# Optimization experiments

Measured on AMD Instinct MI355X. Metric: run time of the kernel, lower is better.

Reference implementation:

```python
import jax, jax.numpy as jnp
import numpy as np

NUM_HEADS = 12


def get_rel_pos(q_size, k_size, rel_pos):
    # rel_pos: (2*max(q,k)-1, C). Here q_size==k_size so no interpolation needed.
    q_coords = jnp.arange(q_size)[:, None] * max(k_size / q_size, 1.0)
    k_coords = jnp.arange(k_size)[None, :] * max(q_size / k_size, 1.0)
    rel = (q_coords - k_coords) + (k_size - 1) * max(q_size / k_size, 1.0)
    return rel_pos[rel.astype(jnp.int32)]  # (q_size, k_size, C)


def add_decomposed_rel_pos(attn, q, rel_pos_h, rel_pos_w, q_size, k_size):
    q_h, q_w = q_size
    k_h, k_w = k_size
    Rh = get_rel_pos(q_h, k_h, rel_pos_h)  # (q_h,k_h,C)
    Rw = get_rel_pos(q_w, k_w, rel_pos_w)  # (q_w,k_w,C)
    B, _, C = q.shape  # B = num_heads * batch
    r_q = q.reshape(B, q_h, q_w, C)
    rel_h = jnp.einsum('bhwc,hkc->bhwk', r_q, Rh)  # (B,q_h,q_w,k_h)
    rel_w = jnp.einsum('bhwc,wkc->bhwk', r_q, Rw)  # (B,q_h,q_w,k_w)
    attn = attn.reshape(B, q_h, q_w, k_h, k_w)
    attn = attn + rel_h[:, :, :, :, None] + rel_w[:, :, :, None, :]
    return attn.reshape(B, q_h * q_w, k_h * k_w)


def setup_inputs() -> dict:
    key = jax.random.key(0)
    ks = jax.random.split(key, 7)
    B, H, W, dim = 128, 14, 14, 768
    head_dim = dim // NUM_HEADS
    return {
        'x': jax.random.normal(ks[0], (B, H, W, dim), dtype=jnp.float32),
        'qkv_w': jax.random.normal(ks[1], (dim, 3 * dim), dtype=jnp.float32) * 0.02,
        'qkv_b': jax.random.normal(ks[2], (3 * dim,), dtype=jnp.float32) * 0.02,
        'proj_w': jax.random.normal(ks[3], (dim, dim), dtype=jnp.float32) * 0.02,
        'proj_b': jax.random.normal(ks[4], (dim,), dtype=jnp.float32) * 0.02,
        'rel_pos_h': jax.random.normal(ks[5], (2 * H - 1, head_dim), dtype=jnp.float32) * 0.02,
        'rel_pos_w': jax.random.normal(ks[6], (2 * W - 1, head_dim), dtype=jnp.float32) * 0.02,
    }


def reference(x, qkv_w, qkv_b, proj_w, proj_b, rel_pos_h, rel_pos_w):
    B, H, W, dim = x.shape
    nh = NUM_HEADS
    hd = dim // nh
    scale = hd ** -0.5
    L = H * W
    # qkv projection: (B,H,W,3*dim) -> (3, nh*B, L, hd)
    qkv = x.reshape(B, L, dim) @ qkv_w + qkv_b
    qkv = qkv.reshape(B, L, 3, nh, hd)
    qkv = jnp.transpose(qkv, (2, 3, 0, 1, 4)).reshape(3, nh * B, L, hd)
    q, k, v = qkv[0], qkv[1], qkv[2]
    attn = jnp.einsum('bqc,bkc->bqk', q * scale, k)  # (nh*B, L, L)
    attn = add_decomposed_rel_pos(attn, q, rel_pos_h, rel_pos_w, (H, W), (H, W))
    attn = jax.nn.softmax(attn, axis=-1)
    out = jnp.einsum('bqk,bkc->bqc', attn, v)  # (nh*B, L, hd)
    out = out.reshape(nh, B, H, W, hd)
    out = jnp.transpose(out, (1, 2, 3, 0, 4)).reshape(B, H, W, dim)
    return out @ proj_w + proj_b
```

## Files before the change

kernel.cpp:

```cpp
#include <hip/hip_runtime.h>
#include <stdint.h>

typedef unsigned short u16;
typedef __bf16 bf16x8 __attribute__((ext_vector_type(8)));
typedef u16 u16x8 __attribute__((ext_vector_type(8)));
typedef float f32x4 __attribute__((ext_vector_type(4)));

#define MFMA16(a,b,c) __builtin_amdgcn_mfma_f32_16x16x32_bf16((a),(b),(c),0,0,0)
#define GLOAD16(gp, lp) __builtin_amdgcn_global_load_lds( \
    (const __attribute__((address_space(1))) void*)(gp), \
    (__attribute__((address_space(3))) void*)(lp), 16, 0, 0)

__device__ __forceinline__ u16 f2bf(float f) {
  union { float f; uint32_t u; } v; v.f = f;
  return (u16)((v.u + 0x7FFFu + ((v.u >> 16) & 1u)) >> 16);
}
__device__ __forceinline__ float bits2f(uint32_t u) {
  union { uint32_t u; float f; } v; v.u = u; return v.f;
}

__global__ void k_cvt(const float* __restrict__ in, u16* __restrict__ out, int n4) {
  int i = blockIdx.x * 256 + threadIdx.x;
  int stride = gridDim.x * 256;
  for (; i < n4; i += stride) {
    float4 v = reinterpret_cast<const float4*>(in)[i];
    ushort4 o;
    o.x = f2bf(v.x); o.y = f2bf(v.y); o.z = f2bf(v.z); o.w = f2bf(v.w);
    reinterpret_cast<ushort4*>(out)[i] = o;
  }
}

__global__ void k_transpose(const float* __restrict__ in, u16* __restrict__ out, int R, int C) {
  __shared__ float t[32][33];
  int tx = threadIdx.x & 31, ty = threadIdx.x >> 5;
  int c0 = blockIdx.x * 32, r0 = blockIdx.y * 32;
  #pragma unroll
  for (int i = 0; i < 4; i++)
    t[ty + i*8][tx] = in[(size_t)(r0 + ty + i*8) * C + (c0 + tx)];
  __syncthreads();
  #pragma unroll
  for (int i = 0; i < 4; i++)
    out[(size_t)(c0 + ty + i*8) * R + (r0 + tx)] = f2bf(t[tx][ty + i*8]);
}

template<int KDIM>
__device__ __forceinline__ void gemm_core(
    const u16* __restrict__ A, const u16* __restrict__ BT,
    int mt, int nt, f32x4 acc[4][4], u16* As, u16* Bs)
{
  int tid = threadIdx.x, lane = tid & 63, w = tid >> 6;
  int g = lane >> 4, c4 = lane & 15;
  int wr = w >> 1, wc = w & 1;
  int srow = lane >> 2;
  int pslot = (lane & 3) ^ ((lane >> 3) & 3);
  int rsel = g ^ ((c4 >> 1) & 3);
  const size_t abase = (size_t)(mt * 128) * KDIM;
  const size_t bbase = (size_t)(nt * 128) * KDIM;
  for (int kt = 0; kt < KDIM / 32; kt++) {
    __syncthreads();
    #pragma unroll
    for (int cc = 0; cc < 2; cc++) {
      int cid = w * 2 + cc;
      int row = cid * 16 + srow;
      GLOAD16(A + abase + (size_t)row * KDIM + kt * 32 + pslot * 8, As + cid * 512);
      GLOAD16(BT + bbase + (size_t)row * KDIM + kt * 32 + pslot * 8, Bs + cid * 512);
    }
    __syncthreads();
    bf16x8 af[4], bfv[4];
    #pragma unroll
    for (int f = 0; f < 4; f++) {
      af[f]  = *(const bf16x8*)(As + (wr * 64 + f * 16 + c4) * 32 + rsel * 8);
      bfv[f] = *(const bf16x8*)(Bs + (wc * 64 + f * 16 + c4) * 32 + rsel * 8);
    }
    #pragma unroll
    for (int fr = 0; fr < 4; fr++)
      #pragma unroll
      for (int fc = 0; fc < 4; fc++)
        acc[fr][fc] = MFMA16(af[fr], bfv[fc], acc[fr][fc]);
  }
}

__global__ __launch_bounds__(256, 3) void k_qkv_gemm(
    const u16* __restrict__ A, const u16* __restrict__ BT, const float* __restrict__ bias,
    u16* __restrict__ qo, u16* __restrict__ ko, u16* __restrict__ vo)
{
  __shared__ u16 As[128 * 32], Bs[128 * 32];
  int bid = blockIdx.x;
  int nt = bid % 18, mt = bid / 18;
  f32x4 z = {0.f, 0.f, 0.f, 0.f};
  f32x4 acc[4][4];
  #pragma unroll
  for (int i = 0; i < 4; i++)
    #pragma unroll
    for (int j = 0; j < 4; j++) acc[i][j] = z;
  gemm_core<768>(A, BT, mt, nt, acc, As, Bs);

  int tid = threadIdx.x, lane = tid & 63, w = tid >> 6;
  int g = lane >> 4, c4 = lane & 15;
  int wr = w >> 1, wc = w & 1;

  u16* dstA[4]; int ccA[4]; float bsA[4]; int hbA[4];
  #pragma unroll
  for (int fc = 0; fc < 4; fc++) {
    int n0 = nt * 128 + wc * 64 + fc * 16;
    int i3 = n0 / 768;
    int r = n0 - i3 * 768;
    dstA[fc] = (i3 == 0) ? qo : (i3 == 1) ? ko : vo;
    hbA[fc] = (r >> 6) * 128;
    ccA[fc] = (r & 63) + c4;
    bsA[fc] = bias[n0 + c4];
  }
  #pragma unroll
  for (int fr = 0; fr < 4; fr++) {
    #pragma unroll
    for (int j = 0; j < 4; j++) {
      int m = mt * 128 + wr * 64 + fr * 16 + g * 4 + j;
      int bb = m / 196;
      int ll = m - bb * 196;
      #pragma unroll
      for (int fc = 0; fc < 4; fc++) {
        dstA[fc][(size_t)((hbA[fc] + bb) * 196 + ll) * 64 + ccA[fc]] =
            f2bf(acc[fr][fc][j] + bsA[fc]);
      }
    }
  }
}

__global__ __launch_bounds__(256, 3) void k_proj_gemm(
    const u16* __restrict__ A, const u16* __restrict__ BT, const float* __restrict__ bias,
    float* __restrict__ out)
{
  __shared__ u16 As[128 * 32], Bs[128 * 32];
  int bid = blockIdx.x;
  int nt = bid % 6, mt = bid / 6;
  f32x4 z = {0.f, 0.f, 0.f, 0.f};
  f32x4 acc[4][4];
  #pragma unroll
  for (int i = 0; i < 4; i++)
    #pragma unroll
    for (int j = 0; j < 4; j++) acc[i][j] = z;
  gemm_core<768>(A, BT, mt, nt, acc, As, Bs);

  int tid = threadIdx.x, lane = tid & 63, w = tid >> 6;
  int g = lane >> 4, c4 = lane & 15;
  int wr = w >> 1, wc = w & 1;
  #pragma unroll
  for (int fc = 0; fc < 4; fc++) {
    int n0 = nt * 128 + wc * 64 + fc * 16 + c4;
    float bs = bias[n0];
    #pragma unroll
    for (int fr = 0; fr < 4; fr++)
      #pragma unroll
      for (int j = 0; j < 4; j++) {
        int m = mt * 128 + wr * 64 + fr * 16 + g * 4 + j;
        out[(size_t)m * 768 + n0] = acc[fr][fc][j] + bs;
      }
  }
}

#define KP 72
#define VP 216
#define PP 136

template<int NT, int KT0, int NMF, int KOFS>
__device__ __forceinline__ void attn_chunk(
    const u16* Kl, const u16* VT, u16* Pw,
    bf16x8 qa0, bf16x8 qa1,
    const uint32_t* ph, const uint32_t* pw,
    const int* qh, const int* qw,
    float* m_run, float* l_run, f32x4* O,
    int g, int c4, int lane)
{
  f32x4 z = {0.f, 0.f, 0.f, 0.f};
  f32x4 S[NT];
  #pragma unroll
  for (int i = 0; i < NT; i++) {
    int key = (KT0 + i) * 16 + c4;
    bf16x8 kb0 = *(const bf16x8*)(Kl + key * KP + g * 8);
    bf16x8 kb1 = *(const bf16x8*)(Kl + key * KP + 32 + g * 8);
    S[i] = MFMA16(qa1, kb1, MFMA16(qa0, kb0, z));
  }
  #pragma unroll
  for (int i = 0; i < NT; i++) {
    int kglob = (KT0 + i) * 16 + c4;
    int kh = kglob / 14;
    int kw = kglob - kh * 14;
    bool valid = (kglob < 196);
    #pragma unroll
    for (int j = 0; j < 4; j++) {
      int ih = qh[j] - kh + 13;
      int iw = qw[j] - kw + 13;
      uint32_t vh = (uint32_t)__builtin_amdgcn_ds_bpermute(((lane & 48) | (ih & 15)) << 2, (int)ph[j]);
      uint32_t vw = (uint32_t)__builtin_amdgcn_ds_bpermute(((lane & 48) | (iw & 15)) << 2, (int)pw[j]);
      float eh = bits2f((ih >= 16) ? (vh & 0xFFFF0000u) : (vh << 16));
      float ew = bits2f((iw >= 16) ? (vw & 0xFFFF0000u) : (vw << 16));
      float s = S[i][j] * 0.125f + eh + ew;
      S[i][j] = valid ? s : -1e30f;
    }
  }
  #pragma unroll
  for (int j = 0; j < 4; j++) {
    float t = S[0][j];
    #pragma unroll
    for (int i = 1; i < NT; i++) t = fmaxf(t, S[i][j]);
    t = fmaxf(t, __shfl_xor(t, 1));
    t = fmaxf(t, __shfl_xor(t, 2));
    t = fmaxf(t, __shfl_xor(t, 4));
    t = fmaxf(t, __shfl_xor(t, 8));
    float mn = fmaxf(m_run[j], t);
    float corr = __expf(m_run[j] - mn);
    m_run[j] = mn;
    l_run[j] *= corr;
    #pragma unroll
    for (int ct = 0; ct < 4; ct++) O[ct][j] *= corr;
  }
  #pragma unroll
  for (int j = 0; j < 4; j++) {
    int prow = (g * 4 + j) * PP;
    float rs = 0.f;
    #pragma unroll
    for (int i = 0; i < NT; i++) {
      float p = __expf(S[i][j] - m_run[j]);
      rs += p;
      Pw[prow + i * 16 + c4] = f2bf(p);
    }
    if (NT == 7) Pw[prow + 112 + c4] = 0;
    rs += __shfl_xor(rs, 1);
    rs += __shfl_xor(rs, 2);
    rs += __shfl_xor(rs, 4);
    rs += __shfl_xor(rs, 8);
    l_run[j] += rs;
  }
  #pragma unroll
  for (int km = 0; km < NMF; km++) {
    bf16x8 pa = *(const bf16x8*)(Pw + c4 * PP + km * 32 + g * 8);
    #pragma unroll
    for (int ct = 0; ct < 4; ct++) {
      bf16x8 vb = *(const bf16x8*)(VT + (ct * 16 + c4) * VP + KOFS + km * 32 + g * 8);
      O[ct] = MFMA16(pa, vb, O[ct]);
    }
  }
}

__global__ __launch_bounds__(256, 2) void k_attn(
    const u16* __restrict__ Q, const u16* __restrict__ Kg, const u16* __restrict__ Vg,
    const u16* __restrict__ RPH, const u16* __restrict__ RPW, u16* __restrict__ Ows)
{
  __shared__ u16 sm[14976 + 13824 + 8704];
  u16* Kl = sm;
  u16* VT = sm + 14976;
  u16* Pl = sm + 14976 + 13824;

  int bh = blockIdx.x;
  int hh = bh >> 7, bb = bh & 127;
  int tid = threadIdx.x, lane = tid & 63, w = tid >> 6;
  int g = lane >> 4, c4 = lane & 15;

  const u16* kbase = Kg + (size_t)bh * (196 * 64);
  const u16* vbase = Vg + (size_t)bh * (196 * 64);
  const u16* qbase = Q + (size_t)bh * (196 * 64);

  for (int ch = tid; ch < 1568; ch += 256) {
    int row = ch >> 3, slot = ch & 7;
    int4 val = *reinterpret_cast<const int4*>(kbase + row * 64 + slot * 8);
    *reinterpret_cast<int4*>(Kl + row * KP + slot * 8) = val;
  }
  for (int i2 = tid; i2 < 12 * KP; i2 += 256) Kl[196 * KP + i2] = 0;
  for (int ch = tid; ch < 784; ch += 256) {
    int kp = ch >> 3, cb = ch & 7;
    int key = kp * 2, cz = cb * 8;
    u16x8 a = *(const u16x8*)(vbase + key * 64 + cz);
    u16x8 b2 = *(const u16x8*)(vbase + (key + 1) * 64 + cz);
    #pragma unroll
    for (int j = 0; j < 8; j++) {
      uint32_t pk = (uint32_t)a[j] | ((uint32_t)b2[j] << 16);
      *reinterpret_cast<uint32_t*>(VT + (cz + j) * VP + key) = pk;
    }
  }
  for (int i2 = tid; i2 < 64 * 20; i2 += 256) {
    int chn = i2 / 20, col = 196 + (i2 - chn * 20);
    VT[chn * VP + col] = 0;
  }
  __syncthreads();

  u16* Pw = Pl + w * (16 * PP);

  for (int qt = w; qt < 13; qt += 4) {
    int qrow = qt * 16 + c4; if (qrow > 195) qrow = 195;
    const u16* qp = qbase + qrow * 64 + g * 8;
    bf16x8 qa0 = *(const bf16x8*)(qp);
    bf16x8 qa1 = *(const bf16x8*)(qp + 32);

    int t1 = 16 + c4; if (t1 > 26) t1 = 26;
    f32x4 z = {0.f, 0.f, 0.f, 0.f};
    f32x4 Eh0 = MFMA16(qa0, *(const bf16x8*)(RPH + c4 * 64 + g * 8), z);
    Eh0 = MFMA16(qa1, *(const bf16x8*)(RPH + c4 * 64 + 32 + g * 8), Eh0);
    f32x4 Eh1 = MFMA16(qa0, *(const bf16x8*)(RPH + t1 * 64 + g * 8), z);
    Eh1 = MFMA16(qa1, *(const bf16x8*)(RPH + t1 * 64 + 32 + g * 8), Eh1);
    f32x4 Ew0 = MFMA16(qa0, *(const bf16x8*)(RPW + c4 * 64 + g * 8), z);
    Ew0 = MFMA16(qa1, *(const bf16x8*)(RPW + c4 * 64 + 32 + g * 8), Ew0);
    f32x4 Ew1 = MFMA16(qa0, *(const bf16x8*)(RPW + t1 * 64 + g * 8), z);
    Ew1 = MFMA16(qa1, *(const bf16x8*)(RPW + t1 * 64 + 32 + g * 8), Ew1);

    uint32_t ph[4], pw[4];
    int qh[4], qw[4];
    #pragma unroll
    for (int j = 0; j < 4; j++) {
      ph[j] = (uint32_t)f2bf(Eh0[j]) | ((uint32_t)f2bf(Eh1[j]) << 16);
      pw[j] = (uint32_t)f2bf(Ew0[j]) | ((uint32_t)f2bf(Ew1[j]) << 16);
      int qi = qt * 16 + g * 4 + j;
      qh[j] = qi / 14;
      qw[j] = qi - qh[j] * 14;
    }

    float m_run[4] = {-3e38f, -3e38f, -3e38f, -3e38f};
    float l_run[4] = {0.f, 0.f, 0.f, 0.f};
    f32x4 O[4] = {z, z, z, z};

    attn_chunk<7, 0, 4, 0>(Kl, VT, Pw, qa0, qa1, ph, pw, qh, qw, m_run, l_run, O, g, c4, lane);
    attn_chunk<6, 7, 3, 112>(Kl, VT, Pw, qa0, qa1, ph, pw, qh, qw, m_run, l_run, O, g, c4, lane);

    #pragma unroll
    for (int j = 0; j < 4; j++) {
      int qi = qt * 16 + g * 4 + j;
      if (qi < 196) {
        float inv = 1.f / l_run[j];
        size_t base = (size_t)(bb * 196 + qi) * 768 + hh * 64;
        #pragma unroll
        for (int ct = 0; ct < 4; ct++)
          Ows[base + ct * 16 + c4] = f2bf(O[ct][j] * inv);
      }
    }
  }
}

extern "C" void kernel_launch(void* const* d_in, const int* in_sizes, int n_in,
                              void* d_out, int out_size, void* d_ws, size_t ws_size,
                              hipStream_t stream) {
  (void)in_sizes; (void)n_in; (void)out_size; (void)ws_size;
  const float* x      = (const float*)d_in[0];
  const float* qkv_w  = (const float*)d_in[1];
  const float* qkv_b  = (const float*)d_in[2];
  const float* proj_w = (const float*)d_in[3];
  const float* proj_b = (const float*)d_in[4];
  const float* rph    = (const float*)d_in[5];
  const float* rpw    = (const float*)d_in[6];
  float* out = (float*)d_out;
  char* ws = (char*)d_ws;

  u16* xb   = (u16*)(ws);
  u16* wT   = (u16*)(ws + 38535168);
  u16* pT   = (u16*)(ws + 42074112);
  u16* rphb = (u16*)(ws + 43253760);
  u16* rpwb = (u16*)(ws + 43257856);
  u16* qws  = (u16*)(ws + 43261952);
  u16* kws  = (u16*)(ws + 81797120);
  u16* vws  = (u16*)(ws + 120332288);
  u16* Ows  = xb;

  k_cvt<<<2048, 256, 0, stream>>>(x, xb, 4816896);
  k_cvt<<<2, 256, 0, stream>>>(rph, rphb, 432);
  k_cvt<<<2, 256, 0, stream>>>(rpw, rpwb, 432);
  k_transpose<<<dim3(72, 24), 256, 0, stream>>>(qkv_w, wT, 768, 2304);
  k_transpose<<<dim3(24, 24), 256, 0, stream>>>(proj_w, pT, 768, 768);
  k_qkv_gemm<<<196 * 18, 256, 0, stream>>>(xb, wT, qkv_b, qws, kws, vws);
  k_attn<<<1536, 256, 0, stream>>>(qws, kws, vws, rphb, rpwb, Ows);
  k_proj_gemm<<<196 * 6, 256, 0, stream>>>(Ows, pT, proj_b, out);
}
```

Before: 313.8 us.

## Restructure attention: fold rel-pos bias into MFMA, transposed S, register P

Rewrites the attention kernel to compute S transposed (keys as rows), folding the decomposed relative-position bias into an extra MFMA using a one-hot key matrix and a per-query rel-pos row in LDS, with the scale pre-applied to K. It drops the online two-chunk softmax for a single-pass max over all 13 key tiles and feeds P straight from registers into the PV MFMA via a permuted V^T layout, removing the LDS P round-trip and the bpermute gathers. K in LDS gets an XOR swizzle, and packed bf16 conversion and vector stores are used for outputs. The QKV and projection GEMMs also remap block indices to change tile scheduling order. In exchange it raises register pressure (13 live S tiles) and rounds the scaled K and the bias to bf16 before use.

```diff
diff --git a/kernel.cpp b/kernel.cpp
--- a/kernel.cpp
+++ b/kernel.cpp
@@ -17,6 +17,19 @@
 }
 __device__ __forceinline__ float bits2f(uint32_t u) {
   union { uint32_t u; float f; } v; v.u = u; return v.f;
+}
+__device__ __forceinline__ uint32_t cvtpk(float lo, float hi) {
+  uint32_t r;
+  asm("v_cvt_pk_bf16_f32 %0, %1, %2" : "=v"(r) : "v"(lo), "v"(hi));
+  return r;
+}
+__device__ __forceinline__ int4 pack8(const u16* v) {
+  int4 r;
+  r.x = (int)((uint32_t)v[0] | ((uint32_t)v[1] << 16));
+  r.y = (int)((uint32_t)v[2] | ((uint32_t)v[3] << 16));
+  r.z = (int)((uint32_t)v[4] | ((uint32_t)v[5] << 16));
+  r.w = (int)((uint32_t)v[6] | ((uint32_t)v[7] << 16));
+  return r;
 }
 
 __global__ void k_cvt(const float* __restrict__ in, u16* __restrict__ out, int n4) {
@@ -85,7 +98,8 @@
     u16* __restrict__ qo, u16* __restrict__ ko, u16* __restrict__ vo)
 {
   __shared__ u16 As[128 * 32], Bs[128 * 32];
-  int bid = blockIdx.x;
+  int bid0 = blockIdx.x;
+  int bid = (bid0 & 7) * 441 + (bid0 >> 3);
   int nt = bid % 18, mt = bid / 18;
   f32x4 z = {0.f, 0.f, 0.f, 0.f};
   f32x4 acc[4][4];
@@ -131,7 +145,8 @@
     float* __restrict__ out)
 {
   __shared__ u16 As[128 * 32], Bs[128 * 32];
-  int bid = blockIdx.x;
+  int bid0 = blockIdx.x;
+  int bid = (bid0 & 7) * 147 + (bid0 >> 3);
   int nt = bid % 6, mt = bid / 6;
   f32x4 z = {0.f, 0.f, 0.f, 0.f};
   f32x4 acc[4][4];
@@ -155,90 +170,6 @@
         int m = mt * 128 + wr * 64 + fr * 16 + g * 4 + j;
         out[(size_t)m * 768 + n0] = acc[fr][fc][j] + bs;
       }
-  }
-}
-
-#define KP 72
-#define VP 216
-#define PP 136
-
-template<int NT, int KT0, int NMF, int KOFS>
-__device__ __forceinline__ void attn_chunk(
-    const u16* Kl, const u16* VT, u16* Pw,
-    bf16x8 qa0, bf16x8 qa1,
-    const uint32_t* ph, const uint32_t* pw,
-    const int* qh, const int* qw,
-    float* m_run, float* l_run, f32x4* O,
-    int g, int c4, int lane)
-{
-  f32x4 z = {0.f, 0.f, 0.f, 0.f};
-  f32x4 S[NT];
-  #pragma unroll
-  for (int i = 0; i < NT; i++) {
-    int key = (KT0 + i) * 16 + c4;
-    bf16x8 kb0 = *(const bf16x8*)(Kl + key * KP + g * 8);
-    bf16x8 kb1 = *(const bf16x8*)(Kl + key * KP + 32 + g * 8);
-    S[i] = MFMA16(qa1, kb1, MFMA16(qa0, kb0, z));
-  }
-  #pragma unroll
-  for (int i = 0; i < NT; i++) {
-    int kglob = (KT0 + i) * 16 + c4;
-    int kh = kglob / 14;
-    int kw = kglob - kh * 14;
-    bool valid = (kglob < 196);
-    #pragma unroll
-    for (int j = 0; j < 4; j++) {
-      int ih = qh[j] - kh + 13;
-      int iw = qw[j] - kw + 13;
-      uint32_t vh = (uint32_t)__builtin_amdgcn_ds_bpermute(((lane & 48) | (ih & 15)) << 2, (int)ph[j]);
-      uint32_t vw = (uint32_t)__builtin_amdgcn_ds_bpermute(((lane & 48) | (iw & 15)) << 2, (int)pw[j]);
-      float eh = bits2f((ih >= 16) ? (vh & 0xFFFF0000u) : (vh << 16));
-      float ew = bits2f((iw >= 16) ? (vw & 0xFFFF0000u) : (vw << 16));
-      float s = S[i][j] * 0.125f + eh + ew;
-      S[i][j] = valid ? s : -1e30f;
-    }
-  }
-  #pragma unroll
-  for (int j = 0; j < 4; j++) {
-    float t = S[0][j];
-    #pragma unroll
-    for (int i = 1; i < NT; i++) t = fmaxf(t, S[i][j]);
-    t = fmaxf(t, __shfl_xor(t, 1));
-    t = fmaxf(t, __shfl_xor(t, 2));
-    t = fmaxf(t, __shfl_xor(t, 4));
-    t = fmaxf(t, __shfl_xor(t, 8));
-    float mn = fmaxf(m_run[j], t);
-    float corr = __expf(m_run[j] - mn);
-    m_run[j] = mn;
-    l_run[j] *= corr;
-    #pragma unroll
-    for (int ct = 0; ct < 4; ct++) O[ct][j] *= corr;
-  }
-  #pragma unroll
-  for (int j = 0; j < 4; j++) {
-    int prow = (g * 4 + j) * PP;
-    float rs = 0.f;
-    #pragma unroll
-    for (int i = 0; i < NT; i++) {
-      float p = __expf(S[i][j] - m_run[j]);
-      rs += p;
-      Pw[prow + i * 16 + c4] = f2bf(p);
-    }
-    if (NT == 7) Pw[prow + 112 + c4] = 0;
-    rs += __shfl_xor(rs, 1);
-    rs += __shfl_xor(rs, 2);
-    rs += __shfl_xor(rs, 4);
-    rs += __shfl_xor(rs, 8);
-    l_run[j] += rs;
-  }
-  #pragma unroll
-  for (int km = 0; km < NMF; km++) {
-    bf16x8 pa = *(const bf16x8*)(Pw + c4 * PP + km * 32 + g * 8);
-    #pragma unroll
-    for (int ct = 0; ct < 4; ct++) {
-      bf16x8 vb = *(const bf16x8*)(VT + (ct * 16 + c4) * VP + KOFS + km * 32 + g * 8);
-      O[ct] = MFMA16(pa, vb, O[ct]);
-    }
   }
 }
 
@@ -246,89 +177,191 @@
     const u16* __restrict__ Q, const u16* __restrict__ Kg, const u16* __restrict__ Vg,
     const u16* __restrict__ RPH, const u16* __restrict__ RPW, u16* __restrict__ Ows)
 {
-  __shared__ u16 sm[14976 + 13824 + 8704];
-  u16* Kl = sm;
-  u16* VT = sm + 14976;
-  u16* Pl = sm + 14976 + 13824;
+  __shared__ u16 K64[208 * 64];
+  __shared__ u16 Krel[208 * 40];
+  __shared__ u16 VT[64 * 232];
+  __shared__ u16 Qrel[4][16 * 40];
 
   int bh = blockIdx.x;
   int hh = bh >> 7, bb = bh & 127;
   int tid = threadIdx.x, lane = tid & 63, w = tid >> 6;
   int g = lane >> 4, c4 = lane & 15;
 
-  const u16* kbase = Kg + (size_t)bh * (196 * 64);
-  const u16* vbase = Vg + (size_t)bh * (196 * 64);
-  const u16* qbase = Q + (size_t)bh * (196 * 64);
-
-  for (int ch = tid; ch < 1568; ch += 256) {
-    int row = ch >> 3, slot = ch & 7;
-    int4 val = *reinterpret_cast<const int4*>(kbase + row * 64 + slot * 8);
-    *reinterpret_cast<int4*>(Kl + row * KP + slot * 8) = val;
-  }
-  for (int i2 = tid; i2 < 12 * KP; i2 += 256) Kl[196 * KP + i2] = 0;
-  for (int ch = tid; ch < 784; ch += 256) {
-    int kp = ch >> 3, cb = ch & 7;
+  const u16* kbase = Kg + (size_t)bh * 12544;
+  const u16* vbase = Vg + (size_t)bh * 12544;
+  const u16* qbase = Q + (size_t)bh * 12544;
+
+  for (int ch = tid; ch < 1664; ch += 256) {
+    int row = ch >> 3, s = ch & 7;
+    u16 outv[8];
+    if (row < 196) {
+      u16x8 v = *(const u16x8*)(kbase + row * 64 + s * 8);
+      #pragma unroll
+      for (int e = 0; e < 8; e++)
+        outv[e] = f2bf(bits2f((uint32_t)v[e] << 16) * 0.125f);
+    } else {
+      #pragma unroll
+      for (int e = 0; e < 8; e++) outv[e] = 0;
+    }
+    *(int4*)(K64 + row * 64 + ((s ^ (row & 7)) * 8)) = pack8(outv);
+  }
+
+  if (tid < 208) {
+    int k = tid;
+    int kh = k / 14, kw2 = k - kh * 14;
+    #pragma unroll
+    for (int s = 0; s < 5; s++) {
+      u16 vals[8];
+      #pragma unroll
+      for (int e = 0; e < 8; e++) {
+        int c = s * 8 + e;
+        u16 x = 0;
+        if (k < 196) {
+          if (c == kh) x = 0x3F80;
+          else if (c == 14 + kw2) x = 0x3F80;
+        } else {
+          if (c == 28) x = 0x3F80;
+        }
+        vals[e] = x;
+      }
+      *(int4*)(Krel + k * 40 + s * 8) = pack8(vals);
+    }
+  }
+
+  for (int i = tid; i < 2048; i += 256) {
+    int chn = i >> 5, c = 192 + (i & 31);
+    if (c >= 196) VT[chn * 232 + c] = 0;
+  }
+  for (int ch2 = tid; ch2 < 784; ch2 += 256) {
+    int kp = ch2 >> 3, cb = ch2 & 7;
     int key = kp * 2, cz = cb * 8;
     u16x8 a = *(const u16x8*)(vbase + key * 64 + cz);
     u16x8 b2 = *(const u16x8*)(vbase + (key + 1) * 64 + cz);
+    int kk = key & 31;
+    int colp = (key >> 5) * 32 + ((kk & 15) >> 2) * 8 + (kk & 3) + ((kk >> 4) << 2);
     #pragma unroll
     for (int j = 0; j < 8; j++) {
       uint32_t pk = (uint32_t)a[j] | ((uint32_t)b2[j] << 16);
-      *reinterpret_cast<uint32_t*>(VT + (cz + j) * VP + key) = pk;
-    }
-  }
-  for (int i2 = tid; i2 < 64 * 20; i2 += 256) {
-    int chn = i2 / 20, col = 196 + (i2 - chn * 20);
-    VT[chn * VP + col] = 0;
+      *(uint32_t*)(VT + (cz + j) * 232 + colp) = pk;
+    }
   }
   __syncthreads();
 
-  u16* Pw = Pl + w * (16 * PP);
+  int t1 = 16 + c4; if (t1 > 26) t1 = 26;
+  bf16x8 rh00 = *(const bf16x8*)(RPH + c4 * 64 + g * 8);
+  bf16x8 rh01 = *(const bf16x8*)(RPH + c4 * 64 + 32 + g * 8);
+  bf16x8 rh10 = *(const bf16x8*)(RPH + t1 * 64 + g * 8);
+  bf16x8 rh11 = *(const bf16x8*)(RPH + t1 * 64 + 32 + g * 8);
+  bf16x8 rw00 = *(const bf16x8*)(RPW + c4 * 64 + g * 8);
+  bf16x8 rw01 = *(const bf16x8*)(RPW + c4 * 64 + 32 + g * 8);
+  bf16x8 rw10 = *(const bf16x8*)(RPW + t1 * 64 + g * 8);
+  bf16x8 rw11 = *(const bf16x8*)(RPW + t1 * 64 + 32 + g * 8);
+
+  f32x4 z4 = {0.f, 0.f, 0.f, 0.f};
 
   for (int qt = w; qt < 13; qt += 4) {
-    int qrow = qt * 16 + c4; if (qrow > 195) qrow = 195;
-    const u16* qp = qbase + qrow * 64 + g * 8;
-    bf16x8 qa0 = *(const bf16x8*)(qp);
-    bf16x8 qa1 = *(const bf16x8*)(qp + 32);
-
-    int t1 = 16 + c4; if (t1 > 26) t1 = 26;
-    f32x4 z = {0.f, 0.f, 0.f, 0.f};
-    f32x4 Eh0 = MFMA16(qa0, *(const bf16x8*)(RPH + c4 * 64 + g * 8), z);
-    Eh0 = MFMA16(qa1, *(const bf16x8*)(RPH + c4 * 64 + 32 + g * 8), Eh0);
-    f32x4 Eh1 = MFMA16(qa0, *(const bf16x8*)(RPH + t1 * 64 + g * 8), z);
-    Eh1 = MFMA16(qa1, *(const bf16x8*)(RPH + t1 * 64 + 32 + g * 8), Eh1);
-    f32x4 Ew0 = MFMA16(qa0, *(const bf16x8*)(RPW + c4 * 64 + g * 8), z);
-    Ew0 = MFMA16(qa1, *(const bf16x8*)(RPW + c4 * 64 + 32 + g * 8), Ew0);
-    f32x4 Ew1 = MFMA16(qa0, *(const bf16x8*)(RPW + t1 * 64 + g * 8), z);
-    Ew1 = MFMA16(qa1, *(const bf16x8*)(RPW + t1 * 64 + 32 + g * 8), Ew1);
-
-    uint32_t ph[4], pw[4];
-    int qh[4], qw[4];
-    #pragma unroll
-    for (int j = 0; j < 4; j++) {
-      ph[j] = (uint32_t)f2bf(Eh0[j]) | ((uint32_t)f2bf(Eh1[j]) << 16);
-      pw[j] = (uint32_t)f2bf(Ew0[j]) | ((uint32_t)f2bf(Ew1[j]) << 16);
-      int qi = qt * 16 + g * 4 + j;
-      qh[j] = qi / 14;
-      qw[j] = qi - qh[j] * 14;
-    }
-
-    float m_run[4] = {-3e38f, -3e38f, -3e38f, -3e38f};
-    float l_run[4] = {0.f, 0.f, 0.f, 0.f};
-    f32x4 O[4] = {z, z, z, z};
-
-    attn_chunk<7, 0, 4, 0>(Kl, VT, Pw, qa0, qa1, ph, pw, qh, qw, m_run, l_run, O, g, c4, lane);
-    attn_chunk<6, 7, 3, 112>(Kl, VT, Pw, qa0, qa1, ph, pw, qh, qw, m_run, l_run, O, g, c4, lane);
-
-    #pragma unroll
-    for (int j = 0; j < 4; j++) {
-      int qi = qt * 16 + g * 4 + j;
-      if (qi < 196) {
-        float inv = 1.f / l_run[j];
-        size_t base = (size_t)(bb * 196 + qi) * 768 + hh * 64;
+    int qi = qt * 16 + c4;
+    int qrow = qi > 195 ? 195 : qi;
+    bf16x8 qa0 = *(const bf16x8*)(qbase + qrow * 64 + g * 8);
+    bf16x8 qa1 = *(const bf16x8*)(qbase + qrow * 64 + 32 + g * 8);
+
+    u16* Qr = (u16*)Qrel[w];
+    {
+      int4 zz = {0, 0, 0, 0};
+      *(int4*)(Qr + lane * 8) = zz;
+      if (lane < 16) *(int4*)(Qr + 512 + lane * 8) = zz;
+      if (g == 0) Qr[c4 * 40 + 28] = f2bf(-30000.f);
+    }
+
+    int qh = qi / 14;
+    int qwv = qi - qh * 14;
+
+    f32x4 e0 = MFMA16(rh00, qa0, z4); e0 = MFMA16(rh01, qa1, e0);
+    f32x4 e1 = MFMA16(rh10, qa0, z4); e1 = MFMA16(rh11, qa1, e1);
+    #pragma unroll
+    for (int tt = 0; tt < 2; tt++) {
+      f32x4 e = tt ? e1 : e0;
+      #pragma unroll
+      for (int j = 0; j < 4; j++) {
+        int t = tt * 16 + 4 * g + j;
+        int kh = qh + 13 - t;
+        if ((unsigned)kh <= 13u) Qr[c4 * 40 + kh] = f2bf(e[j]);
+      }
+    }
+    f32x4 f0 = MFMA16(rw00, qa0, z4); f0 = MFMA16(rw01, qa1, f0);
+    f32x4 f1 = MFMA16(rw10, qa0, z4); f1 = MFMA16(rw11, qa1, f1);
+    #pragma unroll
+    for (int tt = 0; tt < 2; tt++) {
+      f32x4 e = tt ? f1 : f0;
+      #pragma unroll
+      for (int j = 0; j < 4; j++) {
+        int t = tt * 16 + 4 * g + j;
+        int kw3 = qwv + 13 - t;
+        if ((unsigned)kw3 <= 13u) Qr[c4 * 40 + 14 + kw3] = f2bf(e[j]);
+      }
+    }
+
+    bf16x8 qrelB = *(const bf16x8*)(Qr + c4 * 40 + g * 8);
+
+    f32x4 St[13];
+    #pragma unroll
+    for (int i = 0; i < 13; i++) {
+      int key = i * 16 + c4;
+      const u16* kr = K64 + key * 64;
+      int sw = key & 7;
+      bf16x8 kb0 = *(const bf16x8*)(kr + ((g ^ sw) * 8));
+      bf16x8 kb1 = *(const bf16x8*)(kr + (((4 + g) ^ sw) * 8));
+      f32x4 acc = MFMA16(kb0, qa0, z4);
+      acc = MFMA16(kb1, qa1, acc);
+      bf16x8 krl = *(const bf16x8*)(Krel + key * 40 + g * 8);
+      St[i] = MFMA16(krl, qrelB, acc);
+    }
+
+    float mx = -3.0e38f;
+    #pragma unroll
+    for (int i = 0; i < 13; i++)
+      #pragma unroll
+      for (int j = 0; j < 4; j++) mx = fmaxf(mx, St[i][j]);
+    mx = fmaxf(mx, __shfl_xor(mx, 16));
+    mx = fmaxf(mx, __shfl_xor(mx, 32));
+
+    float ls = 0.f;
+    f32x4 O[4] = {z4, z4, z4, z4};
+    #pragma unroll
+    for (int p = 0; p < 7; p++) {
+      float pe[8];
+      #pragma unroll
+      for (int j2 = 0; j2 < 4; j2++) { pe[j2] = __expf(St[2 * p][j2] - mx); ls += pe[j2]; }
+      if (p < 6) {
         #pragma unroll
-        for (int ct = 0; ct < 4; ct++)
-          Ows[base + ct * 16 + c4] = f2bf(O[ct][j] * inv);
+        for (int j2 = 0; j2 < 4; j2++) { pe[4 + j2] = __expf(St[2 * p + 1][j2] - mx); ls += pe[4 + j2]; }
+      } else {
+        #pragma unroll
+        for (int j2 = 0; j2 < 4; j2++) pe[4 + j2] = 0.f;
+      }
+      union { uint32_t u[4]; bf16x8 v; } pb;
+      pb.u[0] = cvtpk(pe[0], pe[1]);
+      pb.u[1] = cvtpk(pe[2], pe[3]);
+      pb.u[2] = cvtpk(pe[4], pe[5]);
+      pb.u[3] = cvtpk(pe[6], pe[7]);
+      #pragma unroll
+      for (int ct = 0; ct < 4; ct++) {
+        bf16x8 va = *(const bf16x8*)(VT + (ct * 16 + c4) * 232 + p * 32 + g * 8);
+        O[ct] = MFMA16(va, pb.v, O[ct]);
+      }
+    }
+    ls += __shfl_xor(ls, 16);
+    ls += __shfl_xor(ls, 32);
+
+    if (qi < 196) {
+      float inv = 1.f / ls;
+      size_t obase = (size_t)(bb * 196 + qi) * 768 + hh * 64;
+      #pragma unroll
+      for (int ct = 0; ct < 4; ct++) {
+        uint32_t o0 = cvtpk(O[ct][0] * inv, O[ct][1] * inv);
+        uint32_t o1 = cvtpk(O[ct][2] * inv, O[ct][3] * inv);
+        uint2 ov = {o0, o1};
+        *(uint2*)(Ows + obase + ct * 16 + g * 4) = ov;
       }
     }
   }
```

Result: faster. 275.3 us (-12.3%).
